# Optimization experiments

Hardware: AMD Instinct MI355X
Metric: run time of the kernel (lower is better)

The kernel has to match this reference:

```python
import jax, jax.numpy as jnp
import numpy as np

B, D_IN, H, C, K, ND = 65536, 1024, 512, 2, 4, 7
LN_EPS = 1e-5
CE_W = jnp.array([0.1, 0.9], dtype=jnp.float32)


def setup_inputs() -> dict:
    key = jax.random.key(0)
    ks = jax.random.split(key, 12)
    x = jax.random.normal(ks[0], (B, D_IN), dtype=jnp.float32)
    labels = jax.random.randint(ks[1], (B,), 0, C)
    domain = jax.random.randint(ks[2], (B,), 0, ND)
    fc1_w = jax.random.normal(ks[3], (120, D_IN), dtype=jnp.float32) / np.sqrt(D_IN)
    fc1_b = jnp.zeros((120,), dtype=jnp.float32)
    fc2_w = jax.random.normal(ks[4], (H, 120), dtype=jnp.float32) / np.sqrt(120)
    fc2_b = jnp.zeros((H,), dtype=jnp.float32)
    ln_g = jnp.ones((H,), dtype=jnp.float32)
    ln_b = jnp.zeros((H,), dtype=jnp.float32)
    sms = 0.1 * jax.random.normal(ks[5], (K + 1, H, C), dtype=jnp.float32)
    sm_biases = 0.1 * jax.random.normal(ks[6], (K + 1, C), dtype=jnp.float32)
    embs = 1e-4 * jax.random.normal(ks[7], (ND, K), dtype=jnp.float32)
    cs_wt = jnp.asarray(0.1, dtype=jnp.float32) + 1e-4 * jax.random.normal(ks[8], (), dtype=jnp.float32)
    return {"x": x, "labels": labels, "domain": domain, "fc1_w": fc1_w, "fc1_b": fc1_b,
            "fc2_w": fc2_w, "fc2_b": fc2_b, "ln_g": ln_g, "ln_b": ln_b,
            "sms": sms, "sm_biases": sm_biases, "embs": embs, "cs_wt": cs_wt}


def _weighted_ce(logits, labels, w):
    # torch CrossEntropyLoss(weight=w): sum_i w[y_i]*nll_i / sum_i w[y_i]
    logp = jax.nn.log_softmax(logits, axis=-1)
    nll = -jnp.take_along_axis(logp, labels[:, None], axis=1)[:, 0]
    wl = w[labels]
    return jnp.sum(wl * nll) / jnp.sum(wl)


def reference(x, labels, domain, fc1_w, fc1_b, fc2_w, fc2_b, ln_g, ln_b, sms, sm_biases, embs, cs_wt):
    h = jax.nn.relu(x @ fc1_w.T + fc1_b)           # [B,120]
    h = jax.nn.relu(h @ fc2_w.T + fc2_b)           # [B,H]
    mu = jnp.mean(h, axis=-1, keepdims=True)
    var = jnp.var(h, axis=-1, keepdims=True)
    h = (h - mu) / jnp.sqrt(var + LN_EPS) * ln_g + ln_b

    # common classifier (expert 0)
    logits_common = h @ sms[0] + sm_biases[0]      # [B,C]

    # domain mixture weights
    dom1h = jax.nn.one_hot(domain, ND, dtype=jnp.float32)
    c_wts = dom1h @ embs                           # [B,K]
    c_wts = jnp.tanh(jnp.concatenate([jnp.full((h.shape[0], 1), 1.0, jnp.float32) * cs_wt, c_wts], axis=1))  # [B,K+1]

    # reordered einsum chain: K+1 small GEMMs then weighted sum (avoids [B,K+1,H] weight tensor)
    per_k = jnp.einsum('bh,khc->bkc', h, sms)      # [B,K+1,C]
    logits_spec = jnp.einsum('bk,bkc->bc', c_wts, per_k) + c_wts @ sm_biases  # [B,C]

    specific_loss = _weighted_ce(logits_spec, labels, CE_W)
    class_loss = _weighted_ce(logits_common, labels, CE_W)

    # orthogonality penalty: per-class gram of expert weight columns vs identity
    cps = jnp.einsum('khc,jhc->ckj', sms, sms)     # [C,K+1,K+1]
    orth_loss = jnp.mean((cps - jnp.eye(K + 1, dtype=jnp.float32)[None]) ** 2)

    loss = class_loss + specific_loss + orth_loss
    return (loss, logits_common, class_loss, specific_loss, orth_loss)
```

## Files before the change

kernel.cpp:

```cpp
#include <hip/hip_runtime.h>
#include <hip/hip_bf16.h>

typedef __attribute__((ext_vector_type(8))) short short8;
typedef __attribute__((ext_vector_type(4))) float floatx4;
typedef __attribute__((ext_vector_type(8))) unsigned short ushort8;

#define BTOT 65536
#define WS_W1BF   0u
#define WS_W2BF   262144u
#define WS_GBF    393216u
#define WS_CONST  409600u
#define WS_H1BF   524288u
#define WS_PART   17301504u

__device__ __forceinline__ unsigned short f2bf(float f) {
  unsigned u = __float_as_uint(f);
  unsigned r = u + 0x7FFFu + ((u >> 16) & 1u);
  return (unsigned short)(r >> 16);
}

__device__ __forceinline__ unsigned cvtpk(float lo, float hi) {
  unsigned r;
  asm("v_cvt_pk_bf16_f32 %0, %1, %2" : "=v"(r) : "v"(lo), "v"(hi));
  return r;
}

__device__ __forceinline__ void gload16(const void* g, void* l) {
  __builtin_amdgcn_global_load_lds(
      (const __attribute__((address_space(1))) unsigned int*)g,
      (__attribute__((address_space(3))) unsigned int*)l, 16, 0, 0);
}

__global__ __launch_bounds__(256) void k0_prep(
    const float* __restrict__ w1, const float* __restrict__ w2,
    const float* __restrict__ ln_g, const float* __restrict__ ln_b,
    const float* __restrict__ sms, const float* __restrict__ smb,
    const float* __restrict__ embs, const float* __restrict__ cs,
    unsigned char* __restrict__ ws) {
  const int blk = blockIdx.x, tid = threadIdx.x;
  if (blk < 32) {
    for (int g = blk * 256 + tid; g < 16384; g += 32 * 256) {
      int ks = g >> 10, d = g & 1023;
      int n = d >> 3, cp = d & 7, c = cp ^ (n & 7);
      ushort8 u;
      if (n < 120) {
        const float* s = w1 + n * 1024 + ks * 64 + c * 8;
        float4 v0 = *(const float4*)s, v1 = *(const float4*)(s + 4);
        u[0] = f2bf(v0.x); u[1] = f2bf(v0.y); u[2] = f2bf(v0.z); u[3] = f2bf(v0.w);
        u[4] = f2bf(v1.x); u[5] = f2bf(v1.y); u[6] = f2bf(v1.z); u[7] = f2bf(v1.w);
      } else {
#pragma unroll
        for (int j = 0; j < 8; ++j) u[j] = 0;
      }
      *(ushort8*)(ws + WS_W1BF + (unsigned)g * 16) = u;
    }
  } else if (blk < 40) {
    for (int g = (blk - 32) * 256 + tid; g < 8192; g += 8 * 256) {
      int lane = g & 63, f = g >> 6;
      int nt = f & 3, ks = (f >> 2) & 3, w = f >> 4;
      int n = w * 64 + nt * 16 + (lane & 15);
      ushort8 u;
#pragma unroll
      for (int j = 0; j < 8; ++j) {
        int khat = ks * 32 + (lane >> 4) * 8 + j;
        int kcol = (khat & 7) * 16 + (khat >> 3);
        u[j] = (kcol < 120) ? f2bf(w2[n * 120 + kcol]) : (unsigned short)0;
      }
      *(ushort8*)(ws + WS_W2BF + (unsigned)g * 16) = u;
    }
  } else if (blk == 40) {
    for (int e = tid; e < 1024; e += 256) {
      int t = e >> 6, lane = e & 63, q = lane & 15;
      ushort8 u;
#pragma unroll
      for (int j = 0; j < 8; ++j) {
        int khat = t * 32 + (lane >> 4) * 8 + j;
        int col = (khat >> 6) * 64 + (khat & 3) * 16 + ((khat >> 2) & 15);
        float v = 0.f;
        if (q < 10) { int kk = q >> 1, c = q & 1; v = ln_g[col] * sms[kk * 1024 + col * 2 + c]; }
        u[j] = f2bf(v);
      }
      *(ushort8*)(ws + WS_GBF + (unsigned)e * 16) = u;
    }
  } else {
    float* cst = (float*)(ws + WS_CONST);
    int lane = tid & 63, w = tid >> 6;
    for (int q = w; q < 10; q += 4) {
      int kk = q >> 1, c = q & 1;
      float s = 0.f;
#pragma unroll
      for (int i = 0; i < 8; ++i) { int k = lane + 64 * i; s += ln_b[k] * sms[kk * 1024 + k * 2 + c]; }
#pragma unroll
      for (int o = 32; o >= 1; o >>= 1) s += __shfl_xor(s, o);
      if (lane == 0) cst[q] = s + smb[kk * 2 + c];
    }
    if (tid == 0) cst[16] = tanhf(cs[0]);
    if (tid < 28) cst[32 + tid] = tanhf(embs[tid]);
  }
}

__global__ __launch_bounds__(512, 2) void k1_gemm1(
    const float* __restrict__ x, const unsigned char* __restrict__ w1bf,
    const float* __restrict__ b1, unsigned char* __restrict__ h1bf) {
  extern __shared__ unsigned char lds[];
  unsigned char* pack = lds + 131072;

  const int tid = threadIdx.x, lane = tid & 63, w = tid >> 6;
  const int l15 = lane & 15, l4 = lane >> 4;
  const int n = w * 16 + l15;
  const float bias = b1[n < 120 ? n : 119];

  short8 bf[32];
#pragma unroll
  for (int f = 0; f < 32; ++f) {
    int ks = f >> 1, ss = f & 1;
    bf[f] = *(const short8*)(w1bf + ks * 16384 + n * 128 +
                             ((ss * 64 + l4 * 16) ^ ((n & 7) << 4)));
  }

  const long xrowbase = (long)blockIdx.x * 256;
  const int srow = tid >> 8;
  const int scol = (tid & 255) * 4;

  float4 st[16];
  {
    const float* src = x + xrowbase * 1024 + (long)tid * 4;
#pragma unroll
    for (int i = 0; i < 16; ++i) st[i] = *(const float4*)(src + i * 2048);
#pragma unroll
    for (int i = 0; i < 16; ++i) {
      int row = i * 2 + srow;
      unsigned off = (unsigned)(row * 2048 + (((scol >> 3) * 16) ^ ((row & 7) << 4)) + (scol & 7) * 2);
      uint2 q;
      q.x = cvtpk(st[i].x, st[i].y);
      q.y = cvtpk(st[i].z, st[i].w);
      *(uint2*)(lds + off) = q;
    }
  }
  asm volatile("s_waitcnt lgkmcnt(0)" ::: "memory");
  __builtin_amdgcn_s_barrier();

  for (int s = 0; s < 8; ++s) {
    const int cur = s & 1;
    if (s < 7) {
      const float* src = x + (xrowbase + (s + 1) * 32) * 1024 + (long)tid * 4;
#pragma unroll
      for (int i = 0; i < 16; ++i) st[i] = *(const float4*)(src + i * 2048);
    }
    __builtin_amdgcn_sched_barrier(0);
    floatx4 acc0 = floatx4{0.f, 0.f, 0.f, 0.f};
    floatx4 acc1 = floatx4{0.f, 0.f, 0.f, 0.f};
    const unsigned char* Xc = lds + cur * 65536;
    const unsigned abase = (unsigned)(l15 * 2048);
#pragma unroll
    for (int kk = 0; kk < 32; ++kk) {
      unsigned ko = (unsigned)((kk * 64 + l4 * 16) ^ ((l15 & 7) << 4));
      short8 a0 = *(const short8*)(Xc + abase + ko);
      short8 a1 = *(const short8*)(Xc + abase + 32768 + ko);
      acc0 = __builtin_amdgcn_mfma_f32_16x16x32_bf16(a0, bf[kk], acc0, 0, 0, 0);
      acc1 = __builtin_amdgcn_mfma_f32_16x16x32_bf16(a1, bf[kk], acc1, 0, 0, 0);
    }
    __builtin_amdgcn_sched_barrier(0);
    if (s < 7) {
      unsigned char* base = lds + (cur ^ 1) * 65536;
#pragma unroll
      for (int i = 0; i < 16; ++i) {
        int row = i * 2 + srow;
        unsigned off = (unsigned)(row * 2048 + (((scol >> 3) * 16) ^ ((row & 7) << 4)) + (scol & 7) * 2);
        uint2 q;
        q.x = cvtpk(st[i].x, st[i].y);
        q.y = cvtpk(st[i].z, st[i].w);
        *(uint2*)(base + off) = q;
      }
    }
#pragma unroll
    for (int mt = 0; mt < 2; ++mt)
#pragma unroll
      for (int r = 0; r < 4; ++r) {
        int row = mt * 16 + l4 * 4 + r;
        float v = (mt ? acc1[r] : acc0[r]) + bias;
        v = v > 0.f ? v : 0.f;
        if (n >= 120) v = 0.f;
        *(unsigned short*)(pack + row * 256 + ((l15 * 16) ^ ((row & 7) << 4)) + w * 2) = f2bf(v);
      }
    asm volatile("s_waitcnt lgkmcnt(0)" ::: "memory");
    __builtin_amdgcn_s_barrier();
    {
      float4 q = *(const float4*)(pack + tid * 16);
      *(float4*)(h1bf + (xrowbase + s * 32) * 256 + tid * 16) = q;
    }
    asm volatile("s_waitcnt lgkmcnt(0)" ::: "memory");
    __builtin_amdgcn_s_barrier();
  }
}

__global__ __launch_bounds__(512, 4) void k2_fused(
    const unsigned char* __restrict__ h1bf, const unsigned char* __restrict__ w2f,
    const unsigned char* __restrict__ gbf, const float* __restrict__ cst,
    const float* __restrict__ b2, const int* __restrict__ labels,
    const int* __restrict__ domain, float* __restrict__ out,
    float* __restrict__ partials) {
  extern __shared__ unsigned char lds[];
  unsigned char* h1s = lds;
  unsigned char* h2s = lds;
  float* stats = (float*)(lds + 65536);
  float* musig = (float*)(lds + 70656);
  float* Af    = (float*)(lds + 71168);

  const int tid = threadIdx.x, lane = tid & 63, w = tid >> 6;
  const int l15 = lane & 15, l4 = lane >> 4;
  const long row0 = (long)blockIdx.x * 64;
  const int n0 = w * 64;

  {
    const unsigned char* hs = h1bf + (long)blockIdx.x * 16384 + w * 2048 + lane * 16;
    gload16(hs, h1s + w * 2048);
    gload16(hs + 1024, h1s + w * 2048 + 1024);
  }
  float b2v[4];
#pragma unroll
  for (int nt = 0; nt < 4; ++nt) b2v[nt] = b2[n0 + nt * 16 + l15];
  __syncthreads();

  floatx4 acc[4][4];
#pragma unroll
  for (int i = 0; i < 4; ++i)
#pragma unroll
    for (int j = 0; j < 4; ++j) acc[i][j] = floatx4{0.f, 0.f, 0.f, 0.f};
#pragma unroll
  for (int ks = 0; ks < 4; ++ks) {
    short8 a[4], b[4];
#pragma unroll
    for (int nt = 0; nt < 4; ++nt)
      b[nt] = *(const short8*)(w2f + (((w * 4 + ks) * 4 + nt) * 64 + lane) * 16);
#pragma unroll
    for (int mt = 0; mt < 4; ++mt) {
      int r = mt * 16 + l15;
      a[mt] = *(const short8*)(h1s + r * 256 + ((ks * 64 + l4 * 16) ^ ((r & 7) << 4)));
    }
#pragma unroll
    for (int mt = 0; mt < 4; ++mt)
#pragma unroll
      for (int nt = 0; nt < 4; ++nt)
        acc[mt][nt] = __builtin_amdgcn_mfma_f32_16x16x32_bf16(a[mt], b[nt], acc[mt][nt], 0, 0, 0);
  }

#pragma unroll
  for (int mt = 0; mt < 4; ++mt)
#pragma unroll
    for (int nt = 0; nt < 4; ++nt)
#pragma unroll
      for (int r = 0; r < 4; ++r) {
        float v = acc[mt][nt][r] + b2v[nt];
        acc[mt][nt][r] = v > 0.f ? v : 0.f;
      }
#pragma unroll
  for (int mt = 0; mt < 4; ++mt)
#pragma unroll
    for (int r = 0; r < 4; ++r) {
      float s = 0.f, q2 = 0.f;
#pragma unroll
      for (int nt = 0; nt < 4; ++nt) { float v = acc[mt][nt][r]; s += v; q2 += v * v; }
#pragma unroll
      for (int o = 1; o <= 8; o <<= 1) { s += __shfl_xor(s, o); q2 += __shfl_xor(q2, o); }
      if (l15 == 0) {
        int row = mt * 16 + l4 * 4 + r;
        stats[row * 20 + w * 2] = s;
        stats[row * 20 + w * 2 + 1] = q2;
      }
    }
  __syncthreads();

  if (tid < 64) {
    float S = 0.f, Q = 0.f;
#pragma unroll
    for (int j = 0; j < 8; ++j) { S += stats[tid * 20 + j * 2]; Q += stats[tid * 20 + j * 2 + 1]; }
    float mu = S * (1.f / 512.f);
    float var = Q * (1.f / 512.f) - mu * mu;
    musig[tid * 2] = mu;
    musig[tid * 2 + 1] = rsqrtf(var + 1e-5f);
  }
  __syncthreads();

#pragma unroll
  for (int mt = 0; mt < 4; ++mt)
#pragma unroll
    for (int r = 0; r < 4; ++r) {
      int row = mt * 16 + l4 * 4 + r;
      float mu = musig[row * 2], rs = musig[row * 2 + 1];
      uint2 qq;
      qq.x = cvtpk((acc[mt][0][r] - mu) * rs, (acc[mt][1][r] - mu) * rs);
      qq.y = cvtpk((acc[mt][2][r] - mu) * rs, (acc[mt][3][r] - mu) * rs);
      *(uint2*)(h2s + row * 1024 + ((w * 128 + l15 * 8) ^ ((row & 7) << 4))) = qq;
    }
  __syncthreads();

  if (w < 4) {
    floatx4 a3 = floatx4{0.f, 0.f, 0.f, 0.f};
    int row = w * 16 + l15;
#pragma unroll
    for (int t = 0; t < 16; ++t) {
      short8 aa = *(const short8*)(h2s + row * 1024 + ((t * 64 + l4 * 16) ^ ((row & 7) << 4)));
      short8 bb = *(const short8*)(gbf + t * 1024 + lane * 16);
      a3 = __builtin_amdgcn_mfma_f32_16x16x32_bf16(aa, bb, a3, 0, 0, 0);
    }
#pragma unroll
    for (int reg = 0; reg < 4; ++reg) {
      int orow = w * 16 + l4 * 4 + reg;
      if (l15 < 10) Af[orow * 20 + l15] = a3[reg];
    }
  }
  __syncthreads();

  if (tid < 64) {
    long grow = row0 + tid;
    float pd[10];
#pragma unroll
    for (int q = 0; q < 10; ++q) pd[q] = Af[tid * 20 + q] + cst[q];
    int lab = labels[grow], dm = domain[grow];
    float cw0 = cst[16];
    float ls0 = cw0 * pd[0], ls1 = cw0 * pd[1];
#pragma unroll
    for (int kk = 1; kk < 5; ++kk) {
      float c = cst[32 + dm * 4 + kk - 1];
      ls0 += c * pd[kk * 2];
      ls1 += c * pd[kk * 2 + 1];
    }
    float lc0 = pd[0], lc1 = pd[1];
    *(float2*)(out + 1 + grow * 2) = float2{lc0, lc1};
    float m1 = fmaxf(lc0, lc1), n1 = fminf(lc0, lc1);
    float lse1 = m1 + logf(1.f + expf(n1 - m1));
    float nllc = lse1 - (lab ? lc1 : lc0);
    float m2 = fmaxf(ls0, ls1), n2 = fminf(ls0, ls1);
    float lse2 = m2 + logf(1.f + expf(n2 - m2));
    float nlls = lse2 - (lab ? ls1 : ls0);
    float wl = lab ? 0.9f : 0.1f;
    float wsum = wl, scom = wl * nllc, sspec = wl * nlls;
#pragma unroll
    for (int o = 32; o >= 1; o >>= 1) {
      wsum += __shfl_xor(wsum, o);
      scom += __shfl_xor(scom, o);
      sspec += __shfl_xor(sspec, o);
    }
    if (tid == 0) {
      partials[(long)blockIdx.x * 4] = wsum;
      partials[(long)blockIdx.x * 4 + 1] = scom;
      partials[(long)blockIdx.x * 4 + 2] = sspec;
    }
  }
}

__global__ __launch_bounds__(256) void k3_finalize(
    const float* __restrict__ partials, const float* __restrict__ sms,
    float* __restrict__ out) {
  __shared__ float wsums[4][3];
  __shared__ float ow[4];
  const int tid = threadIdx.x;
  const int lane = tid & 63, wid = tid >> 6;
  float sw = 0.f, sc = 0.f, ss = 0.f;
  for (int i = tid; i < 1024; i += 256) {
    sw += partials[i * 4];
    sc += partials[i * 4 + 1];
    ss += partials[i * 4 + 2];
  }
#pragma unroll
  for (int o = 32; o >= 1; o >>= 1) {
    sw += __shfl_xor(sw, o);
    sc += __shfl_xor(sc, o);
    ss += __shfl_xor(ss, o);
  }
  if (lane == 0) { wsums[wid][0] = sw; wsums[wid][1] = sc; wsums[wid][2] = ss; }

  float osum = 0.f;
  for (int p = wid; p < 50; p += 4) {
    int c = p / 25, kk = (p / 5) % 5, j = p % 5;
    float acc = 0.f;
#pragma unroll
    for (int hh = 0; hh < 8; ++hh) {
      int h = lane + 64 * hh;
      acc += sms[kk * 1024 + h * 2 + c] * sms[j * 1024 + h * 2 + c];
    }
#pragma unroll
    for (int o = 32; o >= 1; o >>= 1) acc += __shfl_xor(acc, o);
    float d = acc - ((kk == j) ? 1.f : 0.f);
    osum += d * d;
  }
  if (lane == 0) ow[wid] = osum;
  __syncthreads();
  if (tid == 0) {
    float SW = 0.f, SC = 0.f, SS = 0.f, OS = 0.f;
    for (int w = 0; w < 4; ++w) {
      SW += wsums[w][0]; SC += wsums[w][1]; SS += wsums[w][2]; OS += ow[w];
    }
    float orth = OS * (1.f / 50.f);
    float cls = SC / SW;
    float spec = SS / SW;
    out[0] = cls + spec + orth;
    out[131073] = cls;
    out[131074] = spec;
    out[131075] = orth;
  }
}

extern "C" void kernel_launch(void* const* d_in, const int* in_sizes, int n_in,
                              void* d_out, int out_size, void* d_ws, size_t ws_size,
                              hipStream_t stream) {
  const float* x      = (const float*)d_in[0];
  const int* labels   = (const int*)d_in[1];
  const int* domain   = (const int*)d_in[2];
  const float* fc1_w  = (const float*)d_in[3];
  const float* fc1_b  = (const float*)d_in[4];
  const float* fc2_w  = (const float*)d_in[5];
  const float* fc2_b  = (const float*)d_in[6];
  const float* ln_g   = (const float*)d_in[7];
  const float* ln_b   = (const float*)d_in[8];
  const float* sms    = (const float*)d_in[9];
  const float* sm_b   = (const float*)d_in[10];
  const float* embs   = (const float*)d_in[11];
  const float* cs_wt  = (const float*)d_in[12];
  float* out = (float*)d_out;
  unsigned char* ws = (unsigned char*)d_ws;

  (void)hipFuncSetAttribute((const void*)k1_gemm1,
                            hipFuncAttributeMaxDynamicSharedMemorySize, 139264);
  (void)hipFuncSetAttribute((const void*)k2_fused,
                            hipFuncAttributeMaxDynamicSharedMemorySize, 76800);

  hipLaunchKernelGGL(k0_prep, dim3(42), dim3(256), 0, stream,
                     fc1_w, fc2_w, ln_g, ln_b, sms, sm_b, embs, cs_wt, ws);
  hipLaunchKernelGGL(k1_gemm1, dim3(256), dim3(512), 139264, stream,
                     x, ws + WS_W1BF, fc1_b, ws + WS_H1BF);
  hipLaunchKernelGGL(k2_fused, dim3(BTOT / 64), dim3(512), 76800, stream,
                     ws + WS_H1BF, ws + WS_W2BF, ws + WS_GBF,
                     (const float*)(ws + WS_CONST), fc2_b,
                     labels, domain, out, (float*)(ws + WS_PART));
  hipLaunchKernelGGL(k3_finalize, dim3(1), dim3(256), 0, stream,
                     (const float*)(ws + WS_PART), sms, out);
}
```

Before: 123.4 us.

## Restructure GEMM1 into smaller row tiles with streamed fragment-ordered weights

The first GEMM now processes 64 rows per block instead of 256, launching 1024 blocks. It streams W1 B-fragments from global memory (prepacked in MFMA lane order) with a register double buffer, instead of keeping 32 fragments resident in registers. LDS use drops to a static 72KB, and the h1 writeback is deferred one chunk so it overlaps the next chunk. The goal is better occupancy and load balance with less register pressure, at the cost of re-reading weights per block. k2's launch bounds are also changed from 4 to 2 waves per EU.

After: 131.3 us. +6.4%, slower.

```diff
diff --git a/kernel.cpp b/kernel.cpp
--- a/kernel.cpp
+++ b/kernel.cpp
@@ -40,11 +40,13 @@
   const int blk = blockIdx.x, tid = threadIdx.x;
   if (blk < 32) {
     for (int g = blk * 256 + tid; g < 16384; g += 32 * 256) {
-      int ks = g >> 10, d = g & 1023;
-      int n = d >> 3, cp = d & 7, c = cp ^ (n & 7);
+      int lane = g & 63, fi = g >> 6;
+      int w = fi >> 5, kk = fi & 31;
+      int n = w * 16 + (lane & 15);
+      int kb = kk * 32 + ((lane >> 4) << 3);
       ushort8 u;
       if (n < 120) {
-        const float* s = w1 + n * 1024 + ks * 64 + c * 8;
+        const float* s = w1 + n * 1024 + kb;
         float4 v0 = *(const float4*)s, v1 = *(const float4*)(s + 4);
         u[0] = f2bf(v0.x); u[1] = f2bf(v0.y); u[2] = f2bf(v0.z); u[3] = f2bf(v0.w);
         u[4] = f2bf(v1.x); u[5] = f2bf(v1.y); u[6] = f2bf(v1.z); u[7] = f2bf(v1.w);
@@ -100,101 +102,106 @@
 }
 
 __global__ __launch_bounds__(512, 2) void k1_gemm1(
-    const float* __restrict__ x, const unsigned char* __restrict__ w1bf,
+    const float* __restrict__ x, const unsigned char* __restrict__ w1f,
     const float* __restrict__ b1, unsigned char* __restrict__ h1bf) {
-  extern __shared__ unsigned char lds[];
-  unsigned char* pack = lds + 131072;
-
+  __shared__ unsigned char lds[73728];
   const int tid = threadIdx.x, lane = tid & 63, w = tid >> 6;
   const int l15 = lane & 15, l4 = lane >> 4;
   const int n = w * 16 + l15;
   const float bias = b1[n < 120 ? n : 119];
-
-  short8 bf[32];
-#pragma unroll
-  for (int f = 0; f < 32; ++f) {
-    int ks = f >> 1, ss = f & 1;
-    bf[f] = *(const short8*)(w1bf + ks * 16384 + n * 128 +
-                             ((ss * 64 + l4 * 16) ^ ((n & 7) << 4)));
-  }
-
-  const long xrowbase = (long)blockIdx.x * 256;
-  const int srow = tid >> 8;
-  const int scol = (tid & 255) * 4;
-
-  float4 st[16];
+  const long rowblk = (long)blockIdx.x * 64;
+
+  const int rl0 = tid >> 8;
+  const int col4 = tid & 255;
+  const unsigned char* wfb = w1f + (unsigned)(w * 32) * 1024 + (unsigned)lane * 16;
+
+  float4 st[8];
   {
-    const float* src = x + xrowbase * 1024 + (long)tid * 4;
-#pragma unroll
-    for (int i = 0; i < 16; ++i) st[i] = *(const float4*)(src + i * 2048);
-#pragma unroll
-    for (int i = 0; i < 16; ++i) {
-      int row = i * 2 + srow;
-      unsigned off = (unsigned)(row * 2048 + (((scol >> 3) * 16) ^ ((row & 7) << 4)) + (scol & 7) * 2);
-      uint2 q;
-      q.x = cvtpk(st[i].x, st[i].y);
-      q.y = cvtpk(st[i].z, st[i].w);
-      *(uint2*)(lds + off) = q;
-    }
+    const float* src = x + rowblk * 1024 + (long)tid * 4;
+#pragma unroll
+    for (int i = 0; i < 8; ++i) st[i] = *(const float4*)(src + i * 2048);
+  }
+  asm volatile("s_waitcnt vmcnt(0)" ::: "memory");
+#pragma unroll
+  for (int i = 0; i < 8; ++i) {
+    int rl = rl0 + i * 2;
+    unsigned off = (unsigned)(rl * 2048 + ((col4 * 8) ^ ((rl & 7) << 4)));
+    uint2 q; q.x = cvtpk(st[i].x, st[i].y); q.y = cvtpk(st[i].z, st[i].w);
+    *(uint2*)(lds + off) = q;
   }
   asm volatile("s_waitcnt lgkmcnt(0)" ::: "memory");
   __builtin_amdgcn_s_barrier();
 
-  for (int s = 0; s < 8; ++s) {
-    const int cur = s & 1;
-    if (s < 7) {
-      const float* src = x + (xrowbase + (s + 1) * 32) * 1024 + (long)tid * 4;
-#pragma unroll
-      for (int i = 0; i < 16; ++i) st[i] = *(const float4*)(src + i * 2048);
+#pragma unroll
+  for (int c = 0; c < 4; ++c) {
+    const int cb = c & 1;
+    if (c < 3) {
+      const float* src = x + (rowblk + (c + 1) * 16) * 1024 + (long)tid * 4;
+#pragma unroll
+      for (int i = 0; i < 8; ++i) st[i] = *(const float4*)(src + i * 2048);
     }
     __builtin_amdgcn_sched_barrier(0);
-    floatx4 acc0 = floatx4{0.f, 0.f, 0.f, 0.f};
-    floatx4 acc1 = floatx4{0.f, 0.f, 0.f, 0.f};
-    const unsigned char* Xc = lds + cur * 65536;
-    const unsigned abase = (unsigned)(l15 * 2048);
-#pragma unroll
-    for (int kk = 0; kk < 32; ++kk) {
-      unsigned ko = (unsigned)((kk * 64 + l4 * 16) ^ ((l15 & 7) << 4));
-      short8 a0 = *(const short8*)(Xc + abase + ko);
-      short8 a1 = *(const short8*)(Xc + abase + 32768 + ko);
-      acc0 = __builtin_amdgcn_mfma_f32_16x16x32_bf16(a0, bf[kk], acc0, 0, 0, 0);
-      acc1 = __builtin_amdgcn_mfma_f32_16x16x32_bf16(a1, bf[kk], acc1, 0, 0, 0);
+    if (c > 0) {
+      *(uint2*)(h1bf + (rowblk + (long)(c - 1) * 16) * 256 + tid * 8) =
+          *(const uint2*)(lds + 65536 + ((c - 1) & 1) * 4096 + tid * 8);
     }
     __builtin_amdgcn_sched_barrier(0);
-    if (s < 7) {
-      unsigned char* base = lds + (cur ^ 1) * 65536;
-#pragma unroll
-      for (int i = 0; i < 16; ++i) {
-        int row = i * 2 + srow;
-        unsigned off = (unsigned)(row * 2048 + (((scol >> 3) * 16) ^ ((row & 7) << 4)) + (scol & 7) * 2);
-        uint2 q;
-        q.x = cvtpk(st[i].x, st[i].y);
-        q.y = cvtpk(st[i].z, st[i].w);
-        *(uint2*)(base + off) = q;
-      }
-    }
-#pragma unroll
-    for (int mt = 0; mt < 2; ++mt)
+    floatx4 acc = floatx4{0.f, 0.f, 0.f, 0.f};
+    const unsigned char* Xc = lds + cb * 32768;
+    short8 bcur[4], bnxt[4];
+#pragma unroll
+    for (int i = 0; i < 4; ++i) bcur[i] = *(const short8*)(wfb + i * 1024);
+#pragma unroll
+    for (int g = 0; g < 8; ++g) {
+      if (g < 7) {
+#pragma unroll
+        for (int i = 0; i < 4; ++i)
+          bnxt[i] = *(const short8*)(wfb + ((g + 1) * 4 + i) * 1024);
+      }
+#pragma unroll
+      for (int i = 0; i < 4; ++i) {
+        int kk = g * 4 + i;
+        short8 a = *(const short8*)(Xc + l15 * 2048 +
+                                    ((kk * 64 + l4 * 16) ^ ((l15 & 7) << 4)));
+        acc = __builtin_amdgcn_mfma_f32_16x16x32_bf16(a, bcur[i], acc, 0, 0, 0);
+      }
+#pragma unroll
+      for (int i = 0; i < 4; ++i) bcur[i] = bnxt[i];
+    }
+    if (c < 3) {
+      asm volatile("s_waitcnt vmcnt(0)" ::: "memory");
+#pragma unroll
+      for (int i = 0; i < 8; ++i) {
+        int rl = rl0 + i * 2;
+        unsigned off = (unsigned)((cb ^ 1) * 32768 + rl * 2048 +
+                                  ((col4 * 8) ^ ((rl & 7) << 4)));
+        uint2 q; q.x = cvtpk(st[i].x, st[i].y); q.y = cvtpk(st[i].z, st[i].w);
+        *(uint2*)(lds + off) = q;
+      }
+    }
+    {
+      float v0r[4];
 #pragma unroll
       for (int r = 0; r < 4; ++r) {
-        int row = mt * 16 + l4 * 4 + r;
-        float v = (mt ? acc1[r] : acc0[r]) + bias;
-        v = v > 0.f ? v : 0.f;
-        if (n >= 120) v = 0.f;
-        *(unsigned short*)(pack + row * 256 + ((l15 * 16) ^ ((row & 7) << 4)) + w * 2) = f2bf(v);
-      }
+        float t0 = acc[r] + bias;
+        t0 = t0 > 0.f ? t0 : 0.f;
+        v0r[r] = (n < 120) ? t0 : 0.f;
+      }
+#pragma unroll
+      for (int r = 0; r < 4; ++r) {
+        int row = l4 * 4 + r;
+        *(unsigned short*)(lds + 65536 + cb * 4096 + row * 256 +
+                           ((l15 * 16 + w * 2) ^ ((row & 7) << 4))) = f2bf(v0r[r]);
+      }
+    }
     asm volatile("s_waitcnt lgkmcnt(0)" ::: "memory");
     __builtin_amdgcn_s_barrier();
-    {
-      float4 q = *(const float4*)(pack + tid * 16);
-      *(float4*)(h1bf + (xrowbase + s * 32) * 256 + tid * 16) = q;
-    }
-    asm volatile("s_waitcnt lgkmcnt(0)" ::: "memory");
-    __builtin_amdgcn_s_barrier();
-  }
-}
-
-__global__ __launch_bounds__(512, 4) void k2_fused(
+  }
+  *(uint2*)(h1bf + (rowblk + 48) * 256 + tid * 8) =
+      *(const uint2*)(lds + 65536 + 4096 + tid * 8);
+}
+
+__global__ __launch_bounds__(512, 2) void k2_fused(
     const unsigned char* __restrict__ h1bf, const unsigned char* __restrict__ w2f,
     const unsigned char* __restrict__ gbf, const float* __restrict__ cst,
     const float* __restrict__ b2, const int* __restrict__ labels,
@@ -421,14 +428,12 @@
   float* out = (float*)d_out;
   unsigned char* ws = (unsigned char*)d_ws;
 
-  (void)hipFuncSetAttribute((const void*)k1_gemm1,
-                            hipFuncAttributeMaxDynamicSharedMemorySize, 139264);
   (void)hipFuncSetAttribute((const void*)k2_fused,
                             hipFuncAttributeMaxDynamicSharedMemorySize, 76800);
 
   hipLaunchKernelGGL(k0_prep, dim3(42), dim3(256), 0, stream,
                      fc1_w, fc2_w, ln_g, ln_b, sms, sm_b, embs, cs_wt, ws);
-  hipLaunchKernelGGL(k1_gemm1, dim3(256), dim3(512), 139264, stream,
+  hipLaunchKernelGGL(k1_gemm1, dim3(BTOT / 64), dim3(512), 0, stream,
                      x, ws + WS_W1BF, fc1_b, ws + WS_H1BF);
   hipLaunchKernelGGL(k2_fused, dim3(BTOT / 64), dim3(512), 76800, stream,
                      ws + WS_H1BF, ws + WS_W2BF, ws + WS_GBF,
```
